# Kernel optimization log

Hardware: AMD Instinct MI355X
Metric: run time of the kernel (lower is better)

The kernel has to match this reference:

```python
import jax, jax.numpy as jnp
import numpy as np

DIM = 192
HEADS = 6
HEAD_DIM = DIM // HEADS
WS = 8
SHIFT = WS // 2
B, H, W = 32, 64, 64
EPS = 1e-5


def _rel_pos_index(ws):
    coords = np.stack(np.meshgrid(np.arange(ws), np.arange(ws), indexing='ij'))  # [2,ws,ws]
    cf = coords.reshape(2, -1)  # [2,N]
    rel = cf[:, :, None] - cf[:, None, :]  # [2,N,N]
    rel = rel.transpose(1, 2, 0)
    rel[:, :, 0] += ws - 1
    rel[:, :, 1] += ws - 1
    rel[:, :, 0] *= 2 * ws - 1
    return jnp.asarray(rel.sum(-1))  # [N,N] int32


def _shift_mask(Hp, Wp, ws, shift):
    img = np.zeros((Hp, Wp))
    slices = (slice(0, -ws), slice(-ws, -shift), slice(-shift, None))
    cnt = 0
    for hs in slices:
        for wsl in slices:
            img[hs, wsl] = cnt
            cnt += 1
    m = img.reshape(Hp // ws, ws, Wp // ws, ws).transpose(0, 2, 1, 3).reshape(-1, ws * ws)
    diff = m[:, None, :] - m[:, :, None]
    return jnp.asarray(np.where(diff != 0, -100.0, 0.0).astype(np.float32))  # [nW,N,N]


def _layernorm(x, g, b):
    mu = x.mean(-1, keepdims=True)
    var = ((x - mu) ** 2).mean(-1, keepdims=True)
    return (x - mu) / jnp.sqrt(var + EPS) * g + b


def _win_part(x, ws):
    b, h, w, c = x.shape
    x = x.reshape(b, h // ws, ws, w // ws, ws, c).transpose(0, 1, 3, 2, 4, 5)
    return x.reshape(-1, ws * ws, c)


def _win_rev(win, ws, h, w):
    b = win.shape[0] // (h * w // ws // ws)
    x = win.reshape(b, h // ws, w // ws, ws, ws, -1).transpose(0, 1, 3, 2, 4, 5)
    return x.reshape(b, h, w, -1)


def setup_inputs() -> dict:
    key = jax.random.key(0)
    ks = jax.random.split(key, 6)
    d = DIM
    init = lambda k, shape, scale: jax.random.normal(k, shape, jnp.float32) * scale
    return {
        'x': jax.random.normal(ks[0], (B, H, W, d), jnp.float32),
        'ln1_g': jnp.ones((d,), jnp.float32),
        'ln1_b': jnp.zeros((d,), jnp.float32),
        'qkv_w': init(ks[1], (3 * d, d), 0.02),
        'qkv_b': jnp.zeros((3 * d,), jnp.float32),
        'proj_w': init(ks[2], (d, d), 0.02),
        'proj_b': jnp.zeros((d,), jnp.float32),
        'rel_bias_table': init(ks[3], ((2 * WS - 1) ** 2, HEADS), 0.02),
        'ln2_g': jnp.ones((d,), jnp.float32),
        'ln2_b': jnp.zeros((d,), jnp.float32),
        'mlp_w1': init(ks[4], (4 * d, d), 0.02),
        'mlp_b1': jnp.zeros((4 * d,), jnp.float32),
        'mlp_w2': init(ks[5], (d, 4 * d), 0.02),
        'mlp_b2': jnp.zeros((d,), jnp.float32),
    }


def reference(x, ln1_g, ln1_b, qkv_w, qkv_b, proj_w, proj_b, rel_bias_table, ln2_g, ln2_b, mlp_w1, mlp_b1, mlp_w2, mlp_b2):
    b, h, w, c = x.shape
    N = WS * WS
    shortcut = x
    y = _layernorm(x, ln1_g, ln1_b)
    # shifted window: roll, partition
    y = jnp.roll(y, shift=(-SHIFT, -SHIFT), axis=(1, 2))
    xw = _win_part(y, WS)  # [B_, N, C]
    B_ = xw.shape[0]
    qkv = (xw @ qkv_w.T + qkv_b).reshape(B_, N, 3, HEADS, HEAD_DIM)
    q, k, v = qkv[:, :, 0], qkv[:, :, 1], qkv[:, :, 2]  # [B_, N, H, hd]
    scale = HEAD_DIM ** -0.5
    attn = jnp.einsum('bnhd,bmhd->bhnm', q * scale, k)  # [B_, H, N, N]
    rel = rel_bias_table[_rel_pos_index(WS)]  # [N, N, heads]
    attn = attn + rel.transpose(2, 0, 1)[None]
    mask = _shift_mask(h, w, WS, SHIFT)  # [nW, N, N]
    nW = mask.shape[0]
    attn = attn.reshape(B_ // nW, nW, HEADS, N, N) + mask[None, :, None]
    attn = jax.nn.softmax(attn.reshape(B_, HEADS, N, N), axis=-1)
    out = jnp.einsum('bhnm,bmhd->bnhd', attn, v).reshape(B_, N, c)
    out = out @ proj_w.T + proj_b
    y = _win_rev(out, WS, h, w)
    y = jnp.roll(y, shift=(SHIFT, SHIFT), axis=(1, 2))
    x2 = shortcut + y
    z = _layernorm(x2, ln2_g, ln2_b)
    z = jax.nn.gelu(z @ mlp_w1.T + mlp_b1, approximate=False) @ mlp_w2.T + mlp_b2
    return x2 + z
```

## Files before the change

### kernel.cpp

```cpp
#include <hip/hip_runtime.h>
#include <hip/hip_bf16.h>

typedef __bf16 bf16_t;
typedef __bf16 bf16x4 __attribute__((ext_vector_type(4)));
typedef __bf16 bf16x8 __attribute__((ext_vector_type(8)));
typedef float f32x4 __attribute__((ext_vector_type(4)));

#define MFMA16x16(a, b, c) __builtin_amdgcn_mfma_f32_16x16x32_bf16((a), (b), (c), 0, 0, 0)

constexpr int DIM = 192;
constexpr int NHEAD = 6;
constexpr int NWIN = 2048;
constexpr int WTOK = 64;


__global__ __launch_bounds__(256) void cvt_qkvwf(const float* __restrict__ s, bf16_t* __restrict__ d) {
    const int t = blockIdx.x * 256 + threadIdx.x;
    if (t >= 216 * 64) return;
    const int lane = t & 63, f = t >> 6;
    const int nt = f & 1, kk = (f >> 1) % 6, ph = f / 12;
    const int row = ph * 32 + nt * 16 + (lane & 15);
    const int col = kk * 32 + (lane >> 4) * 8;
    const float* sp = s + row * 192 + col;
    bf16_t* dp = d + (size_t)t * 8;
#pragma unroll
    for (int e = 0; e < 8; ++e) dp[e] = (bf16_t)sp[e];
}

__global__ __launch_bounds__(256) void cvt_projwf(const float* __restrict__ s, bf16_t* __restrict__ d) {
    const int t = blockIdx.x * 256 + threadIdx.x;
    if (t >= 72 * 64) return;
    const int lane = t & 63, f = t >> 6;
    const int nt = f % 3, kk = (f / 3) % 6, wv = f / 18;
    const int row = wv * 48 + nt * 16 + (lane & 15);
    const int col = kk * 32 + (lane >> 4) * 8;
    const float* sp = s + row * 192 + col;
    bf16_t* dp = d + (size_t)t * 8;
#pragma unroll
    for (int e = 0; e < 8; ++e) dp[e] = (bf16_t)sp[e];
}

__global__ __launch_bounds__(256) void cvt_w1f(const float* __restrict__ s, bf16_t* __restrict__ d) {
    const int t = blockIdx.x * 256 + threadIdx.x;
    if (t >= 288 * 64) return;
    const int lane = t & 63, f = t >> 6;
    const int nt = f % 3, kk = (f / 3) % 6, q = f / 18;
    const int wv = q & 3, kc = q >> 2;
    const int row = kc * 192 + wv * 48 + nt * 16 + (lane & 15);
    const int col = kk * 32 + (lane >> 4) * 8;
    const float* sp = s + row * 192 + col;
    bf16_t* dp = d + (size_t)t * 8;
#pragma unroll
    for (int e = 0; e < 8; ++e) dp[e] = (bf16_t)sp[e];
}

__global__ __launch_bounds__(256) void cvt_w2f(const float* __restrict__ s, bf16_t* __restrict__ d) {
    const int t = blockIdx.x * 256 + threadIdx.x;
    if (t >= 288 * 64) return;
    const int lane = t & 63, f = t >> 6;
    const int nt = f % 3, kk = (f / 3) % 6, q = f / 18;
    const int wv = q & 3, kc = q >> 2;
    const int row = wv * 48 + nt * 16 + (lane & 15);
    const int col = kc * 192 + kk * 32 + (lane >> 4) * 8;
    const float* sp = s + row * 768 + col;
    bf16_t* dp = d + (size_t)t * 8;
#pragma unroll
    for (int e = 0; e < 8; ++e) dp[e] = (bf16_t)sp[e];
}

__global__ __launch_bounds__(256) void ln_win_kernel(const float* __restrict__ in,
                                                     const float* __restrict__ g,
                                                     const float* __restrict__ bta,
                                                     bf16_t* __restrict__ ywf) {
    __shared__ bf16_t y_s[64][200];
    const int tid = threadIdx.x, lane = tid & 63, wv = tid >> 6;
    const int win = blockIdx.x;
    const int b_ = win >> 6, hb = (win >> 3) & 7, wb = win & 7;
    const float gv0 = g[lane], gv1 = g[lane + 64], gv2 = g[lane + 128];
    const float bv0 = bta[lane], bv1 = bta[lane + 64], bv2 = bta[lane + 128];
    for (int i = 0; i < 16; ++i) {
        const int n = wv * 16 + i;
        const int th = n >> 3, tw = n & 7;
        const int hh = (hb * 8 + th + 4) & 63;
        const int ww = (wb * 8 + tw + 4) & 63;
        const size_t src = ((size_t)(b_ * 64 + hh) * 64 + ww) * DIM;
        const float v0 = in[src + lane], v1 = in[src + lane + 64], v2 = in[src + lane + 128];
        float sm = v0 + v1 + v2;
        float q = v0 * v0 + v1 * v1 + v2 * v2;
#pragma unroll
        for (int m = 1; m < 64; m <<= 1) {
            sm += __shfl_xor(sm, m);
            q += __shfl_xor(q, m);
        }
        const float mu = sm * (1.0f / DIM);
        const float inv = rsqrtf(q * (1.0f / DIM) - mu * mu + 1e-5f);
        y_s[n][lane]       = (bf16_t)((v0 - mu) * inv * gv0 + bv0);
        y_s[n][lane + 64]  = (bf16_t)((v1 - mu) * inv * gv1 + bv1);
        y_s[n][lane + 128] = (bf16_t)((v2 - mu) * inv * gv2 + bv2);
    }
    __syncthreads();
    bf16_t* dst = ywf + (size_t)win * 12288;
    for (int j = tid; j < 1536; j += 256) {
        const int f = j >> 6, ln = j & 63;
        const int mt = f & 3, kk = f >> 2;
        const int row = mt * 16 + (ln & 15), col = kk * 32 + (ln >> 4) * 8;
        *reinterpret_cast<bf16x8*>(dst + (size_t)j * 8) =
            *reinterpret_cast<const bf16x8*>(&y_s[row][col]);
    }
}

__global__ __launch_bounds__(64, 3) void attn_kernel(const bf16_t* __restrict__ ywf,
                                                     const bf16_t* __restrict__ qkvwf,
                                                     const float* __restrict__ qkvb,
                                                     const float* __restrict__ relb,
                                                     bf16_t* __restrict__ aout) {
    __shared__ bf16_t scr[6400];
    const int lane = threadIdx.x;
    const int l15 = lane & 15, l4 = lane >> 4;
    const int wh = (blockIdx.x & 7) * ((NWIN * NHEAD) >> 3) + (blockIdx.x >> 3);
    const int win = wh / 6;
    const int h = wh - win * 6;
    const bf16_t* ywin = ywf + (size_t)win * 12288;

    bf16_t* tb = scr;
    bf16_t* vtb = scr + 4096;

    f32x4 aQ[4][2] = {}, aK[4][2] = {}, aV[4][2] = {};
#pragma unroll
    for (int kk = 0; kk < 6; ++kk) {
        bf16x8 a[4];
#pragma unroll
        for (int mt = 0; mt < 4; ++mt)
            a[mt] = *reinterpret_cast<const bf16x8*>(ywin + ((kk * 4 + mt) << 9) + lane * 8);
        bf16x8 bq[2], bk2[2], bv[2];
#pragma unroll
        for (int nt = 0; nt < 2; ++nt) {
            bq[nt] = *reinterpret_cast<const bf16x8*>(
                qkvwf + (size_t)(((((h) * 6 + kk) << 1) + nt) << 9) + lane * 8);
            bk2[nt] = *reinterpret_cast<const bf16x8*>(
                qkvwf + (size_t)(((((6 + h) * 6 + kk) << 1) + nt) << 9) + lane * 8);
            bv[nt] = *reinterpret_cast<const bf16x8*>(
                qkvwf + (size_t)(((((12 + h) * 6 + kk) << 1) + nt) << 9) + lane * 8);
        }
#pragma unroll
        for (int mt = 0; mt < 4; ++mt)
#pragma unroll
            for (int nt = 0; nt < 2; ++nt) {
                aQ[mt][nt] = MFMA16x16(a[mt], bq[nt], aQ[mt][nt]);
                aK[mt][nt] = MFMA16x16(a[mt], bk2[nt], aK[mt][nt]);
                aV[mt][nt] = MFMA16x16(a[mt], bv[nt], aV[mt][nt]);
            }
    }

#pragma unroll
    for (int nt = 0; nt < 2; ++nt) {
        const int d = nt * 16 + l15;
        const float bias = qkvb[(12 + h) * 32 + d];
#pragma unroll
        for (int mt = 0; mt < 4; ++mt)
#pragma unroll
            for (int r = 0; r < 4; ++r)
                vtb[d * 72 + mt * 16 + l4 * 4 + r] = (bf16_t)(aV[mt][nt][r] + bias);
    }
#pragma unroll
    for (int nt = 0; nt < 2; ++nt) {
        const int d = nt * 16 + l15;
        const float bias = qkvb[h * 32 + d];
#pragma unroll
        for (int mt = 0; mt < 4; ++mt)
#pragma unroll
            for (int r = 0; r < 4; ++r)
                tb[(mt * 16 + l4 * 4 + r) * 40 + d] =
                    (bf16_t)((aQ[mt][nt][r] + bias) * 0.17677669529663689f);
    }
    bf16x8 aq[4];
#pragma unroll
    for (int mt = 0; mt < 4; ++mt)
        aq[mt] = *reinterpret_cast<const bf16x8*>(&tb[(mt * 16 + l15) * 40 + l4 * 8]);

#pragma unroll
    for (int nt = 0; nt < 2; ++nt) {
        const int d = nt * 16 + l15;
        const float bias = qkvb[(6 + h) * 32 + d];
#pragma unroll
        for (int mt = 0; mt < 4; ++mt)
#pragma unroll
            for (int r = 0; r < 4; ++r)
                tb[(mt * 16 + l4 * 4 + r) * 40 + d] = (bf16_t)(aK[mt][nt][r] + bias);
    }
    bf16x8 bk[4];
#pragma unroll
    for (int nt = 0; nt < 4; ++nt)
        bk[nt] = *reinterpret_cast<const bf16x8*>(&tb[(nt * 16 + l15) * 40 + l4 * 8]);

    f32x4 s[4][4] = {};
#pragma unroll
    for (int mt = 0; mt < 4; ++mt)
#pragma unroll
        for (int nt = 0; nt < 4; ++nt)
            s[mt][nt] = MFMA16x16(aq[mt], bk[nt], s[mt][nt]);

    const int hb = (win >> 3) & 7, wb = win & 7;
    int colc[4], colreg[4];
#pragma unroll
    for (int nt = 0; nt < 4; ++nt) {
        const int m = nt * 16 + l15;
        const int mh = m >> 3, mw = m & 7;
        colc[nt] = mh * 15 + mw;
        const int gh = hb * 8 + mh, gw = wb * 8 + mw;
        const int rh = (gh < 56) ? 0 : ((gh < 60) ? 1 : 2);
        const int rw = (gw < 56) ? 0 : ((gw < 60) ? 1 : 2);
        colreg[nt] = rh * 3 + rw;
    }
#pragma unroll
    for (int mt = 0; mt < 4; ++mt) {
#pragma unroll
        for (int r = 0; r < 4; ++r) {
            const int n = mt * 16 + l4 * 4 + r;
            const int nh = n >> 3, nw = n & 7;
            const int rowc = nh * 15 + nw + 112;
            const int gh = hb * 8 + nh, gw = wb * 8 + nw;
            const int rh = (gh < 56) ? 0 : ((gh < 60) ? 1 : 2);
            const int rw = (gw < 56) ? 0 : ((gw < 60) ? 1 : 2);
            const int rreg = rh * 3 + rw;
            float vals[4];
            float mx = -1e30f;
#pragma unroll
            for (int nt = 0; nt < 4; ++nt) {
                float v = s[mt][nt][r] + relb[(rowc - colc[nt]) * NHEAD + h];
                if (rreg != colreg[nt]) v -= 100.0f;
                vals[nt] = v;
                mx = fmaxf(mx, v);
            }
            mx = fmaxf(mx, __shfl_xor(mx, 1));
            mx = fmaxf(mx, __shfl_xor(mx, 2));
            mx = fmaxf(mx, __shfl_xor(mx, 4));
            mx = fmaxf(mx, __shfl_xor(mx, 8));
            float sum = 0.f;
#pragma unroll
            for (int nt = 0; nt < 4; ++nt) {
                vals[nt] = __expf(vals[nt] - mx);
                sum += vals[nt];
            }
            sum += __shfl_xor(sum, 1);
            sum += __shfl_xor(sum, 2);
            sum += __shfl_xor(sum, 4);
            sum += __shfl_xor(sum, 8);
            const float inv = 1.0f / sum;
            const int nsw = n & 7;
#pragma unroll
            for (int nt = 0; nt < 4; ++nt) {
                const int tk = nt * 16 + l15;
                tb[n * 64 + (((tk >> 3) ^ nsw) << 3) + (tk & 7)] = (bf16_t)(vals[nt] * inv);
            }
        }
    }

    f32x4 o[4][2] = {};
#pragma unroll
    for (int kk = 0; kk < 2; ++kk) {
        bf16x8 a[4], b[2];
#pragma unroll
        for (int mt = 0; mt < 4; ++mt) {
            const int tq = mt * 16 + l15;
            a[mt] = *reinterpret_cast<const bf16x8*>(&tb[tq * 64 + (((kk * 4 + l4) ^ (tq & 7)) << 3)]);
        }
#pragma unroll
        for (int nt = 0; nt < 2; ++nt)
            b[nt] = *reinterpret_cast<const bf16x8*>(&vtb[(nt * 16 + l15) * 72 + kk * 32 + l4 * 8]);
#pragma unroll
        for (int mt = 0; mt < 4; ++mt)
#pragma unroll
            for (int nt = 0; nt < 2; ++nt)
                o[mt][nt] = MFMA16x16(a[mt], b[nt], o[mt][nt]);
    }
    bf16_t* op = aout + (size_t)win * (WTOK * DIM) + h * 32;
#pragma unroll
    for (int mt = 0; mt < 4; ++mt)
#pragma unroll
        for (int nt = 0; nt < 2; ++nt)
#pragma unroll
            for (int r = 0; r < 4; ++r) {
                const int n = mt * 16 + l4 * 4 + r;
                op[n * DIM + nt * 16 + l15] = (bf16_t)o[mt][nt][r];
            }
}

__global__ __launch_bounds__(256) void proj_kernel(const bf16_t* __restrict__ ain,
                                                   const bf16_t* __restrict__ pwf,
                                                   const float* __restrict__ pbias,
                                                   const float* __restrict__ x,
                                                   float* __restrict__ x2) {
    __shared__ bf16_t a_s[64][200];
    const int tid = threadIdx.x;
    const int lane = tid & 63;
    const int wv = tid >> 6;
    const int win = blockIdx.x;
    const int l15 = lane & 15, l4 = lane >> 4;

    const bf16_t* asrc = ain + (size_t)win * (WTOK * DIM);
    for (int i = tid; i < WTOK * DIM / 8; i += 256) {
        const int idx = i * 8;
        *reinterpret_cast<bf16x8*>(&a_s[idx / DIM][idx % DIM]) =
            *reinterpret_cast<const bf16x8*>(asrc + idx);
    }
    __syncthreads();

    const int n0 = wv * 48;
    f32x4 acc[4][3] = {};
    for (int kk = 0; kk < 6; ++kk) {
        const int c0 = kk * 32 + l4 * 8;
        bf16x8 a[4], b[3];
#pragma unroll
        for (int mt = 0; mt < 4; ++mt)
            a[mt] = *reinterpret_cast<const bf16x8*>(&a_s[mt * 16 + l15][c0]);
#pragma unroll
        for (int nt = 0; nt < 3; ++nt)
            b[nt] = *reinterpret_cast<const bf16x8*>(
                pwf + (size_t)(((wv * 6 + kk) * 3 + nt) << 9) + lane * 8);
#pragma unroll
        for (int mt = 0; mt < 4; ++mt)
#pragma unroll
            for (int nt = 0; nt < 3; ++nt)
                acc[mt][nt] = MFMA16x16(a[mt], b[nt], acc[mt][nt]);
    }
    const int b_ = win >> 6, hb = (win >> 3) & 7, wb = win & 7;
#pragma unroll
    for (int mt = 0; mt < 4; ++mt)
#pragma unroll
        for (int r = 0; r < 4; ++r) {
            const int n = mt * 16 + l4 * 4 + r;
            const int th = n >> 3, tw = n & 7;
            const int hh = (hb * 8 + th + 4) & 63;
            const int ww = (wb * 8 + tw + 4) & 63;
            const size_t row = ((size_t)(b_ * 64 + hh) * 64 + ww) * DIM;
#pragma unroll
            for (int nt = 0; nt < 3; ++nt) {
                const int col = n0 + nt * 16 + l15;
                x2[row + col] = acc[mt][nt][r] + pbias[col] + x[row + col];
            }
        }
}

__device__ __forceinline__ float gelu_f(float v) {
    const float x2 = v * v;
    const float inner = fmaf(0.044715f * x2, v, v);
    const float e = __expf(inner * 1.5957691216057308f);
    const float r = __builtin_amdgcn_rcpf(e + 1.0f);
    return v - v * r;
}

__global__ __launch_bounds__(256, 3) void mlp_kernel(const float* __restrict__ g,
                                                     const float* __restrict__ bta,
                                                     const bf16_t* __restrict__ w1f,
                                                     const float* __restrict__ b1,
                                                     const bf16_t* __restrict__ w2f,
                                                     const float* __restrict__ b2,
                                                     float* __restrict__ xout) {
    __shared__ bf16_t z_s[64][200];
    __shared__ bf16_t h_s[64][200];
    const int tid = threadIdx.x, lane = tid & 63, wv = tid >> 6;
    const int l15 = lane & 15, l4 = lane >> 4;
    const size_t t0 = (size_t)blockIdx.x * 64;
    const int n0 = wv * 48;

    {
        const float gv0 = g[lane], gv1 = g[lane + 64], gv2 = g[lane + 128];
        const float bv0 = bta[lane], bv1 = bta[lane + 64], bv2 = bta[lane + 128];
        for (int i = 0; i < 16; ++i) {
            const int n = wv * 16 + i;
            const size_t src = (t0 + n) * DIM;
            const float v0 = xout[src + lane], v1 = xout[src + lane + 64], v2 = xout[src + lane + 128];
            float sm = v0 + v1 + v2;
            float q = v0 * v0 + v1 * v1 + v2 * v2;
#pragma unroll
            for (int m = 1; m < 64; m <<= 1) {
                sm += __shfl_xor(sm, m);
                q += __shfl_xor(q, m);
            }
            const float mu = sm * (1.0f / DIM);
            const float inv = rsqrtf(q * (1.0f / DIM) - mu * mu + 1e-5f);
            z_s[n][lane]       = (bf16_t)((v0 - mu) * inv * gv0 + bv0);
            z_s[n][lane + 64]  = (bf16_t)((v1 - mu) * inv * gv1 + bv1);
            z_s[n][lane + 128] = (bf16_t)((v2 - mu) * inv * gv2 + bv2);
        }
    }
    __syncthreads();

    f32x4 acc_o[4][3] = {};
    for (int kc = 0; kc < 4; ++kc) {
        const int fb = (kc * 4 + wv) * 18;
        f32x4 hacc[4][3] = {};
#pragma unroll
        for (int kk = 0; kk < 6; ++kk) {
            const int c0 = kk * 32 + l4 * 8;
            bf16x8 a[4], b[3];
#pragma unroll
            for (int mt = 0; mt < 4; ++mt)
                a[mt] = *reinterpret_cast<const bf16x8*>(&z_s[mt * 16 + l15][c0]);
#pragma unroll
            for (int nt = 0; nt < 3; ++nt)
                b[nt] = *reinterpret_cast<const bf16x8*>(
                    w1f + (size_t)((fb + kk * 3 + nt) << 9) + lane * 8);
#pragma unroll
            for (int mt = 0; mt < 4; ++mt)
#pragma unroll
                for (int nt = 0; nt < 3; ++nt)
                    hacc[mt][nt] = MFMA16x16(a[mt], b[nt], hacc[mt][nt]);
        }
        __syncthreads();
#pragma unroll
        for (int mt = 0; mt < 4; ++mt)
#pragma unroll
            for (int r = 0; r < 4; ++r) {
                const int n = mt * 16 + l4 * 4 + r;
#pragma unroll
                for (int nt = 0; nt < 3; ++nt) {
                    const int col = n0 + nt * 16 + l15;
                    h_s[n][col] = (bf16_t)gelu_f(hacc[mt][nt][r] + b1[kc * 192 + col]);
                }
            }
        __syncthreads();
#pragma unroll
        for (int kk = 0; kk < 6; ++kk) {
            const int c0 = kk * 32 + l4 * 8;
            bf16x8 a[4], b[3];
#pragma unroll
            for (int mt = 0; mt < 4; ++mt)
                a[mt] = *reinterpret_cast<const bf16x8*>(&h_s[mt * 16 + l15][c0]);
#pragma unroll
            for (int nt = 0; nt < 3; ++nt)
                b[nt] = *reinterpret_cast<const bf16x8*>(
                    w2f + (size_t)((fb + kk * 3 + nt) << 9) + lane * 8);
#pragma unroll
            for (int mt = 0; mt < 4; ++mt)
#pragma unroll
                for (int nt = 0; nt < 3; ++nt)
                    acc_o[mt][nt] = MFMA16x16(a[mt], b[nt], acc_o[mt][nt]);
        }
    }
#pragma unroll
    for (int mt = 0; mt < 4; ++mt)
#pragma unroll
        for (int r = 0; r < 4; ++r) {
            const int n = mt * 16 + l4 * 4 + r;
            const size_t addr = (t0 + n) * DIM;
#pragma unroll
            for (int nt = 0; nt < 3; ++nt) {
                const int col = n0 + nt * 16 + l15;
                xout[addr + col] = acc_o[mt][nt][r] + b2[col] + xout[addr + col];
            }
        }
}

extern "C" void kernel_launch(void* const* d_in, const int* in_sizes, int n_in,
                              void* d_out, int out_size, void* d_ws, size_t ws_size,
                              hipStream_t stream) {
    const float* x      = (const float*)d_in[0];
    const float* ln1_g  = (const float*)d_in[1];
    const float* ln1_b  = (const float*)d_in[2];
    const float* qkv_w  = (const float*)d_in[3];
    const float* qkv_b  = (const float*)d_in[4];
    const float* proj_w = (const float*)d_in[5];
    const float* proj_b = (const float*)d_in[6];
    const float* relb   = (const float*)d_in[7];
    const float* ln2_g  = (const float*)d_in[8];
    const float* ln2_b  = (const float*)d_in[9];
    const float* mlp_w1 = (const float*)d_in[10];
    const float* mlp_b1 = (const float*)d_in[11];
    const float* mlp_w2 = (const float*)d_in[12];
    const float* mlp_b2 = (const float*)d_in[13];
    float* out = (float*)d_out;

    char* ws = (char*)d_ws;
    bf16_t* qkvwf = (bf16_t*)(ws + 0);
    bf16_t* pwf   = (bf16_t*)(ws + 221184);
    bf16_t* w1f   = (bf16_t*)(ws + 294912);
    bf16_t* w2f   = (bf16_t*)(ws + 589824);
    bf16_t* bufA  = (bf16_t*)(ws + 884736);
    bf16_t* bufB  = (bf16_t*)(ws + 884736 + 50331648);

    cvt_qkvwf<<<54, 256, 0, stream>>>(qkv_w, qkvwf);
    cvt_projwf<<<18, 256, 0, stream>>>(proj_w, pwf);
    cvt_w1f<<<72, 256, 0, stream>>>(mlp_w1, w1f);
    cvt_w2f<<<72, 256, 0, stream>>>(mlp_w2, w2f);

    ln_win_kernel<<<NWIN, 256, 0, stream>>>(x, ln1_g, ln1_b, bufA);
    attn_kernel<<<NWIN * NHEAD, 64, 0, stream>>>(bufA, qkvwf, qkv_b, relb, bufB);
    proj_kernel<<<NWIN, 256, 0, stream>>>(bufB, pwf, proj_b, x, out);
    mlp_kernel<<<2048, 256, 0, stream>>>(ln2_g, ln2_b, w1f, mlp_b1, w2f, mlp_b2, out);
}
```

Measured before the change: 336.0 us.

## Split LN2 into its own kernel and restructure MLP for lower registers

Merges the four weight conversion kernels into one launch. Moves the second LayerNorm out of the MLP kernel into a separate kernel that writes MFMA-fragment-ordered bf16 activations to global memory. The MLP then reads A fragments directly from global/L2 and computes the first GEMM one N-tile at a time with fewer live accumulators. This frees the z_s shared buffer and registers so it can target 4 blocks per CU instead of 3. The cost is an extra launch, an extra round trip of the normalized activations through memory, and the z fragments being reloaded three times per chunk.

```diff
diff --git a/kernel.cpp b/kernel.cpp
--- a/kernel.cpp
+++ b/kernel.cpp
@@ -2,7 +2,6 @@
 #include <hip/hip_bf16.h>
 
 typedef __bf16 bf16_t;
-typedef __bf16 bf16x4 __attribute__((ext_vector_type(4)));
 typedef __bf16 bf16x8 __attribute__((ext_vector_type(8)));
 typedef float f32x4 __attribute__((ext_vector_type(4)));
 
@@ -13,57 +12,42 @@
 constexpr int NWIN = 2048;
 constexpr int WTOK = 64;
 
-
-__global__ __launch_bounds__(256) void cvt_qkvwf(const float* __restrict__ s, bf16_t* __restrict__ d) {
+__global__ __launch_bounds__(256) void cvt_all(const float* __restrict__ qkv,
+                                               const float* __restrict__ proj,
+                                               const float* __restrict__ w1,
+                                               const float* __restrict__ w2,
+                                               bf16_t* __restrict__ qkvwf,
+                                               bf16_t* __restrict__ pwf,
+                                               bf16_t* __restrict__ w1f,
+                                               bf16_t* __restrict__ w2f) {
     const int t = blockIdx.x * 256 + threadIdx.x;
-    if (t >= 216 * 64) return;
-    const int lane = t & 63, f = t >> 6;
-    const int nt = f & 1, kk = (f >> 1) % 6, ph = f / 12;
-    const int row = ph * 32 + nt * 16 + (lane & 15);
-    const int col = kk * 32 + (lane >> 4) * 8;
-    const float* sp = s + row * 192 + col;
-    bf16_t* dp = d + (size_t)t * 8;
-#pragma unroll
-    for (int e = 0; e < 8; ++e) dp[e] = (bf16_t)sp[e];
-}
-
-__global__ __launch_bounds__(256) void cvt_projwf(const float* __restrict__ s, bf16_t* __restrict__ d) {
-    const int t = blockIdx.x * 256 + threadIdx.x;
-    if (t >= 72 * 64) return;
-    const int lane = t & 63, f = t >> 6;
-    const int nt = f % 3, kk = (f / 3) % 6, wv = f / 18;
-    const int row = wv * 48 + nt * 16 + (lane & 15);
-    const int col = kk * 32 + (lane >> 4) * 8;
-    const float* sp = s + row * 192 + col;
-    bf16_t* dp = d + (size_t)t * 8;
-#pragma unroll
-    for (int e = 0; e < 8; ++e) dp[e] = (bf16_t)sp[e];
-}
-
-__global__ __launch_bounds__(256) void cvt_w1f(const float* __restrict__ s, bf16_t* __restrict__ d) {
-    const int t = blockIdx.x * 256 + threadIdx.x;
-    if (t >= 288 * 64) return;
-    const int lane = t & 63, f = t >> 6;
-    const int nt = f % 3, kk = (f / 3) % 6, q = f / 18;
-    const int wv = q & 3, kc = q >> 2;
-    const int row = kc * 192 + wv * 48 + nt * 16 + (lane & 15);
-    const int col = kk * 32 + (lane >> 4) * 8;
-    const float* sp = s + row * 192 + col;
-    bf16_t* dp = d + (size_t)t * 8;
-#pragma unroll
-    for (int e = 0; e < 8; ++e) dp[e] = (bf16_t)sp[e];
-}
-
-__global__ __launch_bounds__(256) void cvt_w2f(const float* __restrict__ s, bf16_t* __restrict__ d) {
-    const int t = blockIdx.x * 256 + threadIdx.x;
-    if (t >= 288 * 64) return;
-    const int lane = t & 63, f = t >> 6;
-    const int nt = f % 3, kk = (f / 3) % 6, q = f / 18;
-    const int wv = q & 3, kc = q >> 2;
-    const int row = wv * 48 + nt * 16 + (lane & 15);
-    const int col = kc * 192 + kk * 32 + (lane >> 4) * 8;
-    const float* sp = s + row * 768 + col;
-    bf16_t* dp = d + (size_t)t * 8;
+    const int lane = t & 63;
+    const int r15 = lane & 15, c8 = (lane >> 4) * 8;
+    const float* sp;
+    bf16_t* dp;
+    if (t < 216 * 64) {
+        const int f = t >> 6;
+        const int nt = f & 1, kk = (f >> 1) % 6, ph = f / 12;
+        sp = qkv + (ph * 32 + nt * 16 + r15) * 192 + kk * 32 + c8;
+        dp = qkvwf + (size_t)t * 8;
+    } else if (t < 288 * 64) {
+        const int f = (t >> 6) - 216;
+        const int nt = f % 3, kk = (f / 3) % 6, wv = f / 18;
+        sp = proj + (wv * 48 + nt * 16 + r15) * 192 + kk * 32 + c8;
+        dp = pwf + (size_t)(t - 216 * 64) * 8;
+    } else if (t < 576 * 64) {
+        const int f = (t >> 6) - 288;
+        const int nt = f % 3, kk = (f / 3) % 6, q = f / 18;
+        const int wv = q & 3, kc = q >> 2;
+        sp = w1 + (kc * 192 + wv * 48 + nt * 16 + r15) * 192 + kk * 32 + c8;
+        dp = w1f + (size_t)(t - 288 * 64) * 8;
+    } else {
+        const int f = (t >> 6) - 576;
+        const int nt = f % 3, kk = (f / 3) % 6, q = f / 18;
+        const int wv = q & 3, kc = q >> 2;
+        sp = w2 + (size_t)(wv * 48 + nt * 16 + r15) * 768 + kc * 192 + kk * 32 + c8;
+        dp = w2f + (size_t)(t - 576 * 64) * 8;
+    }
 #pragma unroll
     for (int e = 0; e < 8; ++e) dp[e] = (bf16_t)sp[e];
 }
@@ -109,6 +93,43 @@
     }
 }
 
+__global__ __launch_bounds__(256) void ln2f_kernel(const float* __restrict__ in,
+                                                   const float* __restrict__ g,
+                                                   const float* __restrict__ bta,
+                                                   bf16_t* __restrict__ zf) {
+    __shared__ bf16_t y_s[64][200];
+    const int tid = threadIdx.x, lane = tid & 63, wv = tid >> 6;
+    const size_t t0 = (size_t)blockIdx.x * 64;
+    const float gv0 = g[lane], gv1 = g[lane + 64], gv2 = g[lane + 128];
+    const float bv0 = bta[lane], bv1 = bta[lane + 64], bv2 = bta[lane + 128];
+    for (int i = 0; i < 16; ++i) {
+        const int n = wv * 16 + i;
+        const size_t src = (t0 + n) * DIM;
+        const float v0 = in[src + lane], v1 = in[src + lane + 64], v2 = in[src + lane + 128];
+        float sm = v0 + v1 + v2;
+        float q = v0 * v0 + v1 * v1 + v2 * v2;
+#pragma unroll
+        for (int m = 1; m < 64; m <<= 1) {
+            sm += __shfl_xor(sm, m);
+            q += __shfl_xor(q, m);
+        }
+        const float mu = sm * (1.0f / DIM);
+        const float inv = rsqrtf(q * (1.0f / DIM) - mu * mu + 1e-5f);
+        y_s[n][lane]       = (bf16_t)((v0 - mu) * inv * gv0 + bv0);
+        y_s[n][lane + 64]  = (bf16_t)((v1 - mu) * inv * gv1 + bv1);
+        y_s[n][lane + 128] = (bf16_t)((v2 - mu) * inv * gv2 + bv2);
+    }
+    __syncthreads();
+    bf16_t* dst = zf + (size_t)blockIdx.x * 12288;
+    for (int j = tid; j < 1536; j += 256) {
+        const int f = j >> 6, ln = j & 63;
+        const int mt = f & 3, kk = f >> 2;
+        const int row = mt * 16 + (ln & 15), col = kk * 32 + (ln >> 4) * 8;
+        *reinterpret_cast<bf16x8*>(dst + (size_t)j * 8) =
+            *reinterpret_cast<const bf16x8*>(&y_s[row][col]);
+    }
+}
+
 __global__ __launch_bounds__(64, 3) void attn_kernel(const bf16_t* __restrict__ ywf,
                                                      const bf16_t* __restrict__ qkvwf,
                                                      const float* __restrict__ qkvb,
@@ -350,76 +371,65 @@
     return v - v * r;
 }
 
-__global__ __launch_bounds__(256, 3) void mlp_kernel(const float* __restrict__ g,
-                                                     const float* __restrict__ bta,
+__global__ __launch_bounds__(256, 4) void mlp_kernel(const bf16_t* __restrict__ zf,
                                                      const bf16_t* __restrict__ w1f,
                                                      const float* __restrict__ b1,
                                                      const bf16_t* __restrict__ w2f,
                                                      const float* __restrict__ b2,
                                                      float* __restrict__ xout) {
-    __shared__ bf16_t z_s[64][200];
     __shared__ bf16_t h_s[64][200];
     const int tid = threadIdx.x, lane = tid & 63, wv = tid >> 6;
     const int l15 = lane & 15, l4 = lane >> 4;
     const size_t t0 = (size_t)blockIdx.x * 64;
     const int n0 = wv * 48;
-
-    {
-        const float gv0 = g[lane], gv1 = g[lane + 64], gv2 = g[lane + 128];
-        const float bv0 = bta[lane], bv1 = bta[lane + 64], bv2 = bta[lane + 128];
-        for (int i = 0; i < 16; ++i) {
-            const int n = wv * 16 + i;
-            const size_t src = (t0 + n) * DIM;
-            const float v0 = xout[src + lane], v1 = xout[src + lane + 64], v2 = xout[src + lane + 128];
-            float sm = v0 + v1 + v2;
-            float q = v0 * v0 + v1 * v1 + v2 * v2;
-#pragma unroll
-            for (int m = 1; m < 64; m <<= 1) {
-                sm += __shfl_xor(sm, m);
-                q += __shfl_xor(q, m);
-            }
-            const float mu = sm * (1.0f / DIM);
-            const float inv = rsqrtf(q * (1.0f / DIM) - mu * mu + 1e-5f);
-            z_s[n][lane]       = (bf16_t)((v0 - mu) * inv * gv0 + bv0);
-            z_s[n][lane + 64]  = (bf16_t)((v1 - mu) * inv * gv1 + bv1);
-            z_s[n][lane + 128] = (bf16_t)((v2 - mu) * inv * gv2 + bv2);
-        }
-    }
-    __syncthreads();
+    const bf16_t* ztile = zf + (size_t)blockIdx.x * 12288;
 
     f32x4 acc_o[4][3] = {};
     for (int kc = 0; kc < 4; ++kc) {
         const int fb = (kc * 4 + wv) * 18;
-        f32x4 hacc[4][3] = {};
+        f32x4 h0[4] = {};
 #pragma unroll
         for (int kk = 0; kk < 6; ++kk) {
-            const int c0 = kk * 32 + l4 * 8;
-            bf16x8 a[4], b[3];
+            bf16x8 a[4];
 #pragma unroll
             for (int mt = 0; mt < 4; ++mt)
-                a[mt] = *reinterpret_cast<const bf16x8*>(&z_s[mt * 16 + l15][c0]);
-#pragma unroll
-            for (int nt = 0; nt < 3; ++nt)
-                b[nt] = *reinterpret_cast<const bf16x8*>(
+                a[mt] = *reinterpret_cast<const bf16x8*>(ztile + ((kk * 4 + mt) << 9) + lane * 8);
+            const bf16x8 b0 = *reinterpret_cast<const bf16x8*>(
+                w1f + (size_t)((fb + kk * 3 + 0) << 9) + lane * 8);
+#pragma unroll
+            for (int mt = 0; mt < 4; ++mt)
+                h0[mt] = MFMA16x16(a[mt], b0, h0[mt]);
+        }
+        __syncthreads();
+        {
+            const float bias = b1[kc * 192 + n0 + l15];
+#pragma unroll
+            for (int mt = 0; mt < 4; ++mt)
+#pragma unroll
+                for (int r = 0; r < 4; ++r)
+                    h_s[mt * 16 + l4 * 4 + r][n0 + l15] = (bf16_t)gelu_f(h0[mt][r] + bias);
+        }
+        for (int nt = 1; nt < 3; ++nt) {
+            f32x4 hn[4] = {};
+#pragma unroll
+            for (int kk = 0; kk < 6; ++kk) {
+                bf16x8 a[4];
+#pragma unroll
+                for (int mt = 0; mt < 4; ++mt)
+                    a[mt] = *reinterpret_cast<const bf16x8*>(ztile + ((kk * 4 + mt) << 9) + lane * 8);
+                const bf16x8 bn = *reinterpret_cast<const bf16x8*>(
                     w1f + (size_t)((fb + kk * 3 + nt) << 9) + lane * 8);
 #pragma unroll
+                for (int mt = 0; mt < 4; ++mt)
+                    hn[mt] = MFMA16x16(a[mt], bn, hn[mt]);
+            }
+            const float bias = b1[kc * 192 + n0 + nt * 16 + l15];
+#pragma unroll
             for (int mt = 0; mt < 4; ++mt)
 #pragma unroll
-                for (int nt = 0; nt < 3; ++nt)
-                    hacc[mt][nt] = MFMA16x16(a[mt], b[nt], hacc[mt][nt]);
-        }
-        __syncthreads();
-#pragma unroll
-        for (int mt = 0; mt < 4; ++mt)
-#pragma unroll
-            for (int r = 0; r < 4; ++r) {
-                const int n = mt * 16 + l4 * 4 + r;
-#pragma unroll
-                for (int nt = 0; nt < 3; ++nt) {
-                    const int col = n0 + nt * 16 + l15;
-                    h_s[n][col] = (bf16_t)gelu_f(hacc[mt][nt][r] + b1[kc * 192 + col]);
-                }
-            }
+                for (int r = 0; r < 4; ++r)
+                    h_s[mt * 16 + l4 * 4 + r][n0 + nt * 16 + l15] = (bf16_t)gelu_f(hn[mt][r] + bias);
+        }
         __syncthreads();
 #pragma unroll
         for (int kk = 0; kk < 6; ++kk) {
@@ -480,13 +490,11 @@
     bf16_t* bufA  = (bf16_t*)(ws + 884736);
     bf16_t* bufB  = (bf16_t*)(ws + 884736 + 50331648);
 
-    cvt_qkvwf<<<54, 256, 0, stream>>>(qkv_w, qkvwf);
-    cvt_projwf<<<18, 256, 0, stream>>>(proj_w, pwf);
-    cvt_w1f<<<72, 256, 0, stream>>>(mlp_w1, w1f);
-    cvt_w2f<<<72, 256, 0, stream>>>(mlp_w2, w2f);
+    cvt_all<<<216, 256, 0, stream>>>(qkv_w, proj_w, mlp_w1, mlp_w2, qkvwf, pwf, w1f, w2f);
 
     ln_win_kernel<<<NWIN, 256, 0, stream>>>(x, ln1_g, ln1_b, bufA);
     attn_kernel<<<NWIN * NHEAD, 64, 0, stream>>>(bufA, qkvwf, qkv_b, relb, bufB);
     proj_kernel<<<NWIN, 256, 0, stream>>>(bufB, pwf, proj_b, x, out);
-    mlp_kernel<<<2048, 256, 0, stream>>>(ln2_g, ln2_b, w1f, mlp_b1, w2f, mlp_b2, out);
-}
+    ln2f_kernel<<<2048, 256, 0, stream>>>(out, ln2_g, ln2_b, bufA);
+    mlp_kernel<<<2048, 256, 0, stream>>>(bufA, w1f, mlp_b1, w2f, mlp_b2, out);
+}
```

Measured after the change: 627.5 us. +86.8%, slower.
